# Kernel tuning notes

Measured on AMD Instinct MI355X. Metric: run time of the kernel, lower is better.

The kernel has to match this reference:

```python
import jax, jax.numpy as jnp
import numpy as np

B, S, E = 16, 1024, 512
D = 2 * E            # dim of concatenated embeddings, input to QKV and MLP
H1, H2 = 2048, 1024  # hidden_dims
SCALE = float(1.0 / np.sqrt(E))  # code scales by embedding_dim**0.5 (the init arg, not D)


def setup_inputs() -> dict:
    key = jax.random.key(0)
    k = jax.random.split(key, 12)

    def lin_w(kk, fan_in, fan_out):
        return jax.random.normal(kk, (fan_in, fan_out), jnp.float32) * float(1.0 / np.sqrt(fan_in))

    return {
        "emb1": jax.random.normal(k[0], (B, S, E), jnp.float32),
        "emb2": jax.random.normal(k[1], (B, S, E), jnp.float32),
        # query-row masks; all ones (a 0 would -inf an entire softmax row -> NaN)
        "mask1": jnp.ones((B, S // 2), jnp.int32),
        "mask2": jnp.ones((B, S // 2), jnp.int32),
        "Wq": lin_w(k[2], D, D), "bq": jnp.zeros((D,), jnp.float32),
        "Wk": lin_w(k[3], D, D), "bk": jnp.zeros((D,), jnp.float32),
        "Wv": lin_w(k[4], D, D), "bv": jnp.zeros((D,), jnp.float32),
        "W1": lin_w(k[5], D, H1), "b1": jnp.zeros((H1,), jnp.float32),
        "W2": lin_w(k[6], H1, H2), "b2": jnp.zeros((H2,), jnp.float32),
        "W3": lin_w(k[7], H2, 1), "b3": jnp.zeros((1,), jnp.float32),
    }


def reference(emb1, emb2, mask1, mask2, Wq, bq, Wk, bk, Wv, bv, W1, b1, W2, b2, W3, b3):
    x = jnp.concatenate([emb1, emb2], axis=-1)        # [B, S, D]
    mask = jnp.concatenate([mask1, mask2], axis=-1)   # [B, S] (query-row mask)

    # QKV self-attention with query-only mask
    Q = x @ Wq + bq
    K = x @ Wk + bk
    V = x @ Wv + bv
    scores = jnp.einsum("bqd,bkd->bqk", Q, K) * SCALE  # [B, S, S]
    scores = jnp.where(mask[:, :, None] == 0, -jnp.inf, scores)
    attn = jax.nn.softmax(scores, axis=-1)
    attended = jnp.einsum("bqk,bkd->bqd", attn, V)     # [B, S, D]

    # MLP head (Dropout is identity in eval mode)
    h = jax.nn.relu(attended @ W1 + b1)
    h = jax.nn.relu(h @ W2 + b2)
    logits = h @ W3 + b3                               # [B, S, 1]
    return jax.nn.sigmoid(logits)
```

## Files before the change

### kernel.cpp

```cpp
#include <hip/hip_runtime.h>
#include <math.h>

#define DEV __device__ __forceinline__
#define SB0() __builtin_amdgcn_sched_barrier(0)

typedef unsigned short u16;
typedef unsigned int   u32;
typedef __bf16 bf16x8 __attribute__((ext_vector_type(8)));
typedef float  f32x4  __attribute__((ext_vector_type(4)));
typedef u16    u16x8  __attribute__((ext_vector_type(8)));
typedef u16    u16x4  __attribute__((ext_vector_type(4)));

DEV u16 f2b(float f) {
  u32 u = __builtin_bit_cast(u32, f);
  u = (u + 0x7FFFu + ((u >> 16) & 1u)) >> 16;
  return (u16)u;
}
DEV float b2f(u16 h) { u32 u = (u32)h << 16; return __builtin_bit_cast(float, u); }

DEV void gl_lds16(const u16* g, u16* l) {
  __builtin_amdgcn_global_load_lds((const __attribute__((address_space(1))) void*)g,
                                   (__attribute__((address_space(3))) void*)l, 16, 0, 0);
}

DEV float wred_max(float v) {
#pragma unroll
  for (int o = 32; o > 0; o >>= 1) v = fmaxf(v, __shfl_xor(v, o, 64));
  return v;
}
DEV float wred_sum(float v) {
#pragma unroll
  for (int o = 32; o > 0; o >>= 1) v += __shfl_xor(v, o, 64);
  return v;
}

__global__ __launch_bounds__(256) void concat_convert(
    const float* __restrict__ e1, const float* __restrict__ e2, u16* __restrict__ xb) {
  const size_t idx = ((size_t)blockIdx.x * 256 + threadIdx.x) * 8;
  const int d = (int)(idx & 1023);
  const size_t row = idx >> 10;
  const float* s = (d < 512) ? (e1 + row * 512 + d) : (e2 + row * 512 + (d - 512));
  f32x4 a = *(const f32x4*)s;
  f32x4 b = *(const f32x4*)(s + 4);
  u16x8 o;
  o[0]=f2b(a[0]); o[1]=f2b(a[1]); o[2]=f2b(a[2]); o[3]=f2b(a[3]);
  o[4]=f2b(b[0]); o[5]=f2b(b[1]); o[6]=f2b(b[2]); o[7]=f2b(b[3]);
  *(u16x8*)(xb + idx) = o;
}

__global__ __launch_bounds__(256) void transpose_w(
    const float* __restrict__ W, int ldi, u16* __restrict__ WT, int ldo) {
  __shared__ float tile[64][65];
  const int tx = threadIdx.x & 63, ty = threadIdx.x >> 6;
  const int r0 = blockIdx.y * 64, c0 = blockIdx.x * 64;
#pragma unroll
  for (int i = 0; i < 16; ++i)
    tile[ty + 4*i][tx] = W[(size_t)(r0 + ty + 4*i) * ldi + c0 + tx];
  __syncthreads();
#pragma unroll
  for (int i = 0; i < 16; ++i)
    WT[(size_t)(c0 + ty + 4*i) * ldo + r0 + tx] = f2b(tile[tx][ty + 4*i]);
}

__global__ void concat_bias(const float* __restrict__ bq, const float* __restrict__ bk,
                            float* __restrict__ o) {
  int i = blockIdx.x * 256 + threadIdx.x;
  o[i] = (i < 1024) ? bq[i] : bk[i - 1024];
}

template<int F32OUT, int RELU, int RBIAS>
__global__ __launch_bounds__(512, 2) void gemm256(
    const u16* __restrict__ A, int lda, long long sA,
    const u16* __restrict__ B, int ldb, long long sB,
    void* __restrict__ C, int ldc, long long sC,
    const float* __restrict__ bias, float scale, int K) {
  __shared__ __align__(16) u16 lds[2][2][16384];

  const int t  = threadIdx.x;
  const int ln = t & 63, wv = t >> 6;

  int bx, by, bz;
  {
    const int gx = gridDim.x, gy = gridDim.y, gz = gridDim.z;
    const int nwg = gx * gy * gz;
    const int F = (blockIdx.z * gy + blockIdx.y) * gx + blockIdx.x;
    const int q = nwg >> 3;
    const int L = (F & 7) * q + (F >> 3);
    if (gz > 1) {
      const int pb = gx * gy;
      bz = L / pb; const int r = L - bz * pb;
      by = r / gx; bx = r - by * gx;
    } else {
      bz = 0;
      const int sh = ((gy & 7) == 0) ? 8 : 4;
      const int sw = gx * sh;
      const int sy = L / sw; const int r = L - sy * sw;
      bx = r / sh; by = sy * sh + (r - bx * sh);
    }
  }
  const int m0 = by * 256, n0 = bx * 256;
  A += (size_t)bz * (size_t)sA; B += (size_t)bz * (size_t)sB;

  const int gl = (ln & 7) ^ (ln >> 3);
  const u16* gAs = A + (size_t)(m0 + (t >> 3)) * lda + gl * 8;
  const u16* gBs = B + (size_t)(n0 + (t >> 3)) * ldb + gl * 8;

  const int l15 = ln & 15, lhi = ln >> 4;
  const int wm = (wv >> 2) * 128, wn = (wv & 3) * 64;
  const int colk0 = ((lhi ^ (l15 & 7)) << 3);
  const int colk1 = (((4 + lhi) ^ (l15 & 7)) << 3);
  const int rcA = (wv >> 2) * 8192 + l15 * 64;
  const int rcB = ((wv & 3) >> 1) * 8192 + (wv & 1) * 4096 + l15 * 64;

  f32x4 acc[8][4] = {};
  bf16x8 Af[4][2], Bf[4][2];
  const int KT = K >> 6, NIT = KT >> 1;

#define STG(T, OP, H, LD, GS)                                              \
  if ((T) < KT) {                                                          \
    const u16* _s = (GS) + (size_t)(H) * 128 * (size_t)(LD) + (size_t)(T) * 64; \
    u16* _d = &lds[(T) & 1][OP][(H) * 8192 + wv * 512];                    \
    gl_lds16(_s, _d); gl_lds16(_s + 64 * (size_t)(LD), _d + 4096);         \
  }
#define RDA(BUF, ILO) {                                                    \
  _Pragma("unroll") for (int ii = 0; ii < 4; ++ii) {                       \
    Af[ii][0] = *(const bf16x8*)&lds[BUF][0][rcA + ((ILO) + ii) * 1024 + colk0]; \
    Af[ii][1] = *(const bf16x8*)&lds[BUF][0][rcA + ((ILO) + ii) * 1024 + colk1]; } }
#define RDB(BUF, JLO) {                                                    \
  _Pragma("unroll") for (int jj = 0; jj < 2; ++jj) {                       \
    Bf[(JLO) + jj][0] = *(const bf16x8*)&lds[BUF][1][rcB + ((JLO) + jj) * 1024 + colk0]; \
    Bf[(JLO) + jj][1] = *(const bf16x8*)&lds[BUF][1][rcB + ((JLO) + jj) * 1024 + colk1]; } }
#define MM(ILO, JLO) {                                                     \
  _Pragma("unroll") for (int ii = 0; ii < 4; ++ii)                         \
  _Pragma("unroll") for (int jj = 0; jj < 2; ++jj) {                       \
    acc[(ILO)+ii][(JLO)+jj] = __builtin_amdgcn_mfma_f32_16x16x32_bf16(Af[ii][0], Bf[(JLO)+jj][0], acc[(ILO)+ii][(JLO)+jj], 0, 0, 0); \
    acc[(ILO)+ii][(JLO)+jj] = __builtin_amdgcn_mfma_f32_16x16x32_bf16(Af[ii][1], Bf[(JLO)+jj][1], acc[(ILO)+ii][(JLO)+jj], 0, 0, 0); } }
#define BAR() __builtin_amdgcn_s_barrier()
#define LGKM0() { asm volatile("s_waitcnt lgkmcnt(0)" ::: "memory"); SB0(); }
#define PRIO(x) __builtin_amdgcn_s_setprio(x)

  STG(0, 0, 0, lda, gAs); STG(0, 0, 1, lda, gAs);
  STG(0, 1, 0, ldb, gBs); STG(0, 1, 1, ldb, gBs);
  STG(1, 1, 0, ldb, gBs); STG(1, 1, 1, ldb, gBs);
  asm volatile("s_waitcnt vmcnt(4)" ::: "memory");
  SB0(); BAR();

  for (int it = 0; it < NIT; ++it) {
    const int T0 = it << 1, T1 = T0 + 1;
    RDA(0, 0); RDB(0, 0); STG(T1, 0, 0, lda, gAs);
    asm volatile("s_waitcnt lgkmcnt(8)" ::: "memory"); SB0();
    BAR(); LGKM0();
    PRIO(1); MM(0, 0); PRIO(0); BAR();
    RDB(0, 2); STG(T1, 0, 1, lda, gAs); SB0();
    BAR(); LGKM0();
    PRIO(1); MM(0, 2); PRIO(0); BAR();
    RDA(0, 4); STG(T0 + 2, 1, 0, ldb, gBs); SB0();
    BAR(); LGKM0();
    PRIO(1); MM(4, 0); PRIO(0); BAR();
    STG(T0 + 2, 1, 1, ldb, gBs); SB0();
    BAR();
    PRIO(1); MM(4, 2); PRIO(0);
    if (T0 + 2 < KT) { asm volatile("s_waitcnt vmcnt(4)" ::: "memory"); }
    else             { asm volatile("s_waitcnt vmcnt(0)" ::: "memory"); }
    SB0(); BAR();
    RDA(1, 0); RDB(1, 0); STG(T0 + 2, 0, 0, lda, gAs);
    asm volatile("s_waitcnt lgkmcnt(8)" ::: "memory"); SB0();
    BAR(); LGKM0();
    PRIO(1); MM(0, 0); PRIO(0); BAR();
    RDB(1, 2); STG(T0 + 2, 0, 1, lda, gAs); SB0();
    BAR(); LGKM0();
    PRIO(1); MM(0, 2); PRIO(0); BAR();
    RDA(1, 4); STG(T0 + 3, 1, 0, ldb, gBs); SB0();
    BAR(); LGKM0();
    PRIO(1); MM(4, 0); PRIO(0); BAR();
    STG(T0 + 3, 1, 1, ldb, gBs); SB0();
    BAR();
    PRIO(1); MM(4, 2); PRIO(0);
    if (T0 + 3 < KT) { asm volatile("s_waitcnt vmcnt(4)" ::: "memory"); }
    SB0(); BAR();
  }
#undef STG
#undef RDA
#undef RDB
#undef MM
#undef BAR
#undef LGKM0
#undef PRIO

  const size_t cb = (size_t)bz * (size_t)sC;
#pragma unroll
  for (int i = 0; i < 8; ++i) {
    const int rg = m0 + wm + i * 16 + lhi * 4;
#pragma unroll
    for (int j = 0; j < 4; ++j) {
      const int cg = n0 + wn + j * 16 + l15;
      const float cbv = (!RBIAS && bias) ? bias[cg] : 0.f;
#pragma unroll
      for (int r = 0; r < 4; ++r) {
        float v = acc[i][j][r] * scale + (RBIAS ? bias[rg + r] : cbv);
        if (RELU) v = fmaxf(v, 0.f);
        if (F32OUT) ((float*)C)[cb + (size_t)(rg + r) * ldc + cg] = v;
        else        ((u16*)C)[cb + (size_t)(rg + r) * ldc + cg] = f2b(v);
      }
    }
  }
}

__global__ __launch_bounds__(256) void softmax_mask(
    const float* __restrict__ sc, const int* __restrict__ m1,
    const int* __restrict__ m2, u16* __restrict__ attn) {
  __shared__ float red[8];
  const int row = blockIdx.x;
  const int b = row >> 10, q = row & 1023;
  const int mk = (q < 512) ? m1[b * 512 + q] : m2[b * 512 + q - 512];
  f32x4 v = ((const f32x4*)(sc + (size_t)row * 1024))[threadIdx.x];
  if (mk == 0) { v[0] = v[1] = v[2] = v[3] = -INFINITY; }
  float mx = fmaxf(fmaxf(v[0], v[1]), fmaxf(v[2], v[3]));
  mx = wred_max(mx);
  const int ln = threadIdx.x & 63, wv = threadIdx.x >> 6;
  if (ln == 0) red[wv] = mx;
  __syncthreads();
  mx = fmaxf(fmaxf(red[0], red[1]), fmaxf(red[2], red[3]));
  float e0 = __expf(v[0] - mx), e1 = __expf(v[1] - mx);
  float e2 = __expf(v[2] - mx), e3 = __expf(v[3] - mx);
  float s = wred_sum(e0 + e1 + e2 + e3);
  if (ln == 0) red[4 + wv] = s;
  __syncthreads();
  const float inv = 1.f / (red[4] + red[5] + red[6] + red[7]);
  u16x4 o; o[0] = f2b(e0 * inv); o[1] = f2b(e1 * inv); o[2] = f2b(e2 * inv); o[3] = f2b(e3 * inv);
  *(u16x4*)(attn + (size_t)row * 1024 + threadIdx.x * 4) = o;
}

__global__ __launch_bounds__(256) void logits_sigmoid(
    const u16* __restrict__ h2, const float* __restrict__ W3,
    const float* __restrict__ b3, float* __restrict__ out) {
  const int wid = (blockIdx.x * 256 + threadIdx.x) >> 6;
  const int ln = threadIdx.x & 63;
  const u16* r = h2 + (size_t)wid * 1024 + ln * 16;
  u16x8 v0 = *(const u16x8*)r;
  u16x8 v1 = *(const u16x8*)(r + 8);
  const float* w = W3 + ln * 16;
  float s = 0.f;
#pragma unroll
  for (int i = 0; i < 8; ++i) s += b2f(v0[i]) * w[i];
#pragma unroll
  for (int i = 0; i < 8; ++i) s += b2f(v1[i]) * w[8 + i];
#pragma unroll
  for (int o = 32; o > 0; o >>= 1) s += __shfl_down(s, o, 64);
  if (ln == 0) out[wid] = 1.f / (1.f + __expf(-(s + b3[0])));
}

extern "C" void kernel_launch(void* const* d_in, const int* in_sizes, int n_in,
                              void* d_out, int out_size, void* d_ws, size_t ws_size,
                              hipStream_t stream) {
  (void)in_sizes; (void)n_in; (void)out_size; (void)ws_size;
  const float* emb1 = (const float*)d_in[0];
  const float* emb2 = (const float*)d_in[1];
  const int*   mask1 = (const int*)d_in[2];
  const int*   mask2 = (const int*)d_in[3];
  const float* Wq = (const float*)d_in[4];  const float* bq = (const float*)d_in[5];
  const float* Wk = (const float*)d_in[6];  const float* bk = (const float*)d_in[7];
  const float* Wv = (const float*)d_in[8];  const float* bv = (const float*)d_in[9];
  const float* W1 = (const float*)d_in[10]; const float* b1 = (const float*)d_in[11];
  const float* W2 = (const float*)d_in[12]; const float* b2 = (const float*)d_in[13];
  const float* W3 = (const float*)d_in[14]; const float* b3 = (const float*)d_in[15];

  char* ws = (char*)d_ws;
  u16*  XB    = (u16*)(ws + 0);
  u16*  QK    = (u16*)(ws + 33554432);
  u16*  VT    = (u16*)(ws + 100663296);
  float* SC   = (float*)(ws + 134217728);
  u16*  WTQKV = (u16*)(ws + 201326592);
  u16*  W1T   = (u16*)(ws + 207618048);
  u16*  W2T   = (u16*)(ws + 211812352);
  float* BF_  = (float*)(ws + 216006656);
  u16*  ATTN  = XB;
  u16*  ATT   = (u16*)(ws + 134217728);
  u16*  H1    = QK;
  u16*  H2    = VT;
  float* out  = (float*)d_out;

  const float SCALE = 0.04419417382415922f;

  concat_convert<<<8192, 256, 0, stream>>>(emb1, emb2, XB);
  transpose_w<<<dim3(16, 16), 256, 0, stream>>>(Wq, 1024, WTQKV, 1024);
  transpose_w<<<dim3(16, 16), 256, 0, stream>>>(Wk, 1024, WTQKV + 1024 * 1024, 1024);
  transpose_w<<<dim3(16, 16), 256, 0, stream>>>(Wv, 1024, WTQKV + 2048 * 1024, 1024);
  transpose_w<<<dim3(32, 16), 256, 0, stream>>>(W1, 2048, W1T, 1024);
  transpose_w<<<dim3(16, 32), 256, 0, stream>>>(W2, 1024, W2T, 2048);
  concat_bias<<<8, 256, 0, stream>>>(bq, bk, BF_);

  gemm256<0, 0, 0><<<dim3(8, 64, 1), 512, 0, stream>>>(
      XB, 1024, 0, WTQKV, 1024, 0, QK, 2048, 0, BF_, 1.f, 1024);
  gemm256<0, 0, 1><<<dim3(64, 4, 1), 512, 0, stream>>>(
      WTQKV + 2048 * 1024, 1024, 0, XB, 1024, 0, VT, 16384, 0, bv, 1.f, 1024);
  gemm256<1, 0, 0><<<dim3(4, 4, 16), 512, 0, stream>>>(
      QK, 2048, 2097152LL, QK + 1024, 2048, 2097152LL,
      SC, 1024, 1048576LL, nullptr, SCALE, 1024);
  softmax_mask<<<16384, 256, 0, stream>>>(SC, mask1, mask2, ATTN);
  gemm256<0, 0, 0><<<dim3(4, 4, 16), 512, 0, stream>>>(
      ATTN, 1024, 1048576LL, VT, 16384, 1024LL,
      ATT, 1024, 1048576LL, nullptr, 1.f, 1024);
  gemm256<0, 1, 0><<<dim3(8, 64, 1), 512, 0, stream>>>(
      ATT, 1024, 0, W1T, 1024, 0, H1, 2048, 0, b1, 1.f, 1024);
  gemm256<0, 1, 0><<<dim3(4, 64, 1), 512, 0, stream>>>(
      H1, 2048, 0, W2T, 2048, 0, H2, 1024, 0, b2, 1.f, 2048);
  logits_sigmoid<<<4096, 256, 0, stream>>>(H2, W3, b3, out);
}
```

Baseline: 390.7 us.

## Merge prep kernels into one launch and stage bf16 GEMM epilogue through LDS

Folds the input concat/convert, the five weight transposes and the bias concat into a single prep kernel that branches on block index, cutting six launches and their serialization gaps. Separately, the bf16 GEMM epilogue now writes results into a swizzled per-wave LDS region and then issues 16-byte coalesced global stores instead of scattered 2-byte stores. The epilogue reuses the main-loop LDS buffer without a block barrier, which relies on each wave's region being private and on prior reads having completed.

```diff
diff --git a/kernel.cpp b/kernel.cpp
--- a/kernel.cpp
+++ b/kernel.cpp
@@ -34,25 +34,40 @@
   return v;
 }
 
-__global__ __launch_bounds__(256) void concat_convert(
-    const float* __restrict__ e1, const float* __restrict__ e2, u16* __restrict__ xb) {
-  const size_t idx = ((size_t)blockIdx.x * 256 + threadIdx.x) * 8;
-  const int d = (int)(idx & 1023);
-  const size_t row = idx >> 10;
-  const float* s = (d < 512) ? (e1 + row * 512 + d) : (e2 + row * 512 + (d - 512));
-  f32x4 a = *(const f32x4*)s;
-  f32x4 b = *(const f32x4*)(s + 4);
-  u16x8 o;
-  o[0]=f2b(a[0]); o[1]=f2b(a[1]); o[2]=f2b(a[2]); o[3]=f2b(a[3]);
-  o[4]=f2b(b[0]); o[5]=f2b(b[1]); o[6]=f2b(b[2]); o[7]=f2b(b[3]);
-  *(u16x8*)(xb + idx) = o;
-}
-
-__global__ __launch_bounds__(256) void transpose_w(
-    const float* __restrict__ W, int ldi, u16* __restrict__ WT, int ldo) {
+__global__ __launch_bounds__(256) void prep(
+    const float* __restrict__ e1, const float* __restrict__ e2, u16* __restrict__ xb,
+    const float* __restrict__ Wq, const float* __restrict__ Wk, const float* __restrict__ Wv,
+    const float* __restrict__ W1, const float* __restrict__ W2,
+    u16* __restrict__ WTQKV, u16* __restrict__ W1T, u16* __restrict__ W2T,
+    const float* __restrict__ bq, const float* __restrict__ bk, float* __restrict__ bf) {
   __shared__ float tile[64][65];
+  const int bid = blockIdx.x;
+  if (bid < 8192) {
+    const size_t idx = ((size_t)bid * 256 + threadIdx.x) * 8;
+    const int d = (int)(idx & 1023);
+    const size_t row = idx >> 10;
+    const float* s = (d < 512) ? (e1 + row * 512 + d) : (e2 + row * 512 + (d - 512));
+    f32x4 a = *(const f32x4*)s;
+    f32x4 b = *(const f32x4*)(s + 4);
+    u16x8 o;
+    o[0]=f2b(a[0]); o[1]=f2b(a[1]); o[2]=f2b(a[2]); o[3]=f2b(a[3]);
+    o[4]=f2b(b[0]); o[5]=f2b(b[1]); o[6]=f2b(b[2]); o[7]=f2b(b[3]);
+    *(u16x8*)(xb + idx) = o;
+    return;
+  }
+  if (bid >= 9984) {
+    int i = (bid - 9984) * 256 + threadIdx.x;
+    bf[i] = (i < 1024) ? bq[i] : bk[i - 1024];
+    return;
+  }
+  const float* W; u16* WT; int ldi, ldo, bx, by;
+  if (bid < 8448)      { W = Wq; WT = WTQKV;              ldi = 1024; ldo = 1024; int v = bid - 8192; bx = v & 15; by = v >> 4; }
+  else if (bid < 8704) { W = Wk; WT = WTQKV + 1024*1024;  ldi = 1024; ldo = 1024; int v = bid - 8448; bx = v & 15; by = v >> 4; }
+  else if (bid < 8960) { W = Wv; WT = WTQKV + 2048*1024;  ldi = 1024; ldo = 1024; int v = bid - 8704; bx = v & 15; by = v >> 4; }
+  else if (bid < 9472) { W = W1; WT = W1T;                ldi = 2048; ldo = 1024; int v = bid - 8960; bx = v & 31; by = v >> 5; }
+  else                 { W = W2; WT = W2T;                ldi = 1024; ldo = 2048; int v = bid - 9472; bx = v & 15; by = v >> 4; }
   const int tx = threadIdx.x & 63, ty = threadIdx.x >> 6;
-  const int r0 = blockIdx.y * 64, c0 = blockIdx.x * 64;
+  const int r0 = by * 64, c0 = bx * 64;
 #pragma unroll
   for (int i = 0; i < 16; ++i)
     tile[ty + 4*i][tx] = W[(size_t)(r0 + ty + 4*i) * ldi + c0 + tx];
@@ -60,12 +75,6 @@
 #pragma unroll
   for (int i = 0; i < 16; ++i)
     WT[(size_t)(c0 + ty + 4*i) * ldo + r0 + tx] = f2b(tile[tx][ty + 4*i]);
-}
-
-__global__ void concat_bias(const float* __restrict__ bq, const float* __restrict__ bk,
-                            float* __restrict__ o) {
-  int i = blockIdx.x * 256 + threadIdx.x;
-  o[i] = (i < 1024) ? bq[i] : bk[i - 1024];
 }
 
 template<int F32OUT, int RELU, int RBIAS>
@@ -188,20 +197,50 @@
 #undef PRIO
 
   const size_t cb = (size_t)bz * (size_t)sC;
-#pragma unroll
-  for (int i = 0; i < 8; ++i) {
-    const int rg = m0 + wm + i * 16 + lhi * 4;
-#pragma unroll
-    for (int j = 0; j < 4; ++j) {
-      const int cg = n0 + wn + j * 16 + l15;
-      const float cbv = (!RBIAS && bias) ? bias[cg] : 0.f;
-#pragma unroll
-      for (int r = 0; r < 4; ++r) {
-        float v = acc[i][j][r] * scale + (RBIAS ? bias[rg + r] : cbv);
-        if (RELU) v = fmaxf(v, 0.f);
-        if (F32OUT) ((float*)C)[cb + (size_t)(rg + r) * ldc + cg] = v;
-        else        ((u16*)C)[cb + (size_t)(rg + r) * ldc + cg] = f2b(v);
+  if (F32OUT) {
+#pragma unroll
+    for (int i = 0; i < 8; ++i) {
+      const int rg = m0 + wm + i * 16 + lhi * 4;
+#pragma unroll
+      for (int j = 0; j < 4; ++j) {
+        const int cg = n0 + wn + j * 16 + l15;
+        const float cbv = (!RBIAS && bias) ? bias[cg] : 0.f;
+#pragma unroll
+        for (int r = 0; r < 4; ++r) {
+          float v = acc[i][j][r] * scale + (RBIAS ? bias[rg + r] : cbv);
+          if (RELU) v = fmaxf(v, 0.f);
+          ((float*)C)[cb + (size_t)(rg + r) * ldc + cg] = v;
+        }
       }
+    }
+  } else {
+    u16* ep = ((u16*)lds) + wv * 8192;
+#pragma unroll
+    for (int i = 0; i < 8; ++i) {
+      const int rg = m0 + wm + i * 16 + lhi * 4;
+#pragma unroll
+      for (int j = 0; j < 4; ++j) {
+        const int cg = n0 + wn + j * 16 + l15;
+        const float cbv = (!RBIAS && bias) ? bias[cg] : 0.f;
+#pragma unroll
+        for (int r = 0; r < 4; ++r) {
+          float v = acc[i][j][r] * scale + (RBIAS ? bias[rg + r] : cbv);
+          if (RELU) v = fmaxf(v, 0.f);
+          const int lrow = i * 16 + lhi * 4 + r;
+          const int lcol = (j * 16 + l15) ^ (((lrow >> 2) & 7) << 3);
+          ep[lrow * 64 + lcol] = f2b(v);
+        }
+      }
+    }
+    asm volatile("s_waitcnt lgkmcnt(0)" ::: "memory");
+    SB0();
+    const int l3 = ln >> 3, c0 = (ln & 7) * 8;
+#pragma unroll
+    for (int rep = 0; rep < 16; ++rep) {
+      const int lr = rep * 8 + l3;
+      const int cs = c0 ^ (((lr >> 2) & 7) << 3);
+      u16x8 v = *(const u16x8*)&ep[lr * 64 + cs];
+      *(u16x8*)((u16*)C + cb + (size_t)(m0 + wm + lr) * ldc + n0 + wn + c0) = v;
     }
   }
 }
@@ -282,13 +321,8 @@
 
   const float SCALE = 0.04419417382415922f;
 
-  concat_convert<<<8192, 256, 0, stream>>>(emb1, emb2, XB);
-  transpose_w<<<dim3(16, 16), 256, 0, stream>>>(Wq, 1024, WTQKV, 1024);
-  transpose_w<<<dim3(16, 16), 256, 0, stream>>>(Wk, 1024, WTQKV + 1024 * 1024, 1024);
-  transpose_w<<<dim3(16, 16), 256, 0, stream>>>(Wv, 1024, WTQKV + 2048 * 1024, 1024);
-  transpose_w<<<dim3(32, 16), 256, 0, stream>>>(W1, 2048, W1T, 1024);
-  transpose_w<<<dim3(16, 32), 256, 0, stream>>>(W2, 1024, W2T, 2048);
-  concat_bias<<<8, 256, 0, stream>>>(bq, bk, BF_);
+  prep<<<9992, 256, 0, stream>>>(emb1, emb2, XB, Wq, Wk, Wv, W1, W2,
+                                 WTQKV, W1T, W2T, bq, bk, BF_);
 
   gemm256<0, 0, 0><<<dim3(8, 64, 1), 512, 0, stream>>>(
       XB, 1024, 0, WTQKV, 1024, 0, QK, 2048, 0, BF_, 1.f, 1024);
```

Result: faster. 363.0 us (-7.1%).
